# Kernel tuning notes

Hardware: AMD Instinct MI355X
Metric: run time of the kernel (lower is better)

Reference implementation:

```python
import jax, jax.numpy as jnp
import numpy as np

ALPHA = 0.2  # LeakyReLU negative slope

def setup_inputs() -> dict:
    key = jax.random.key(0)
    k1, k2, k3 = jax.random.split(key, 3)
    B, N, IN_DIM = 16, 1024, 128
    HEADS, HEAD_DIM = 2, 64  # out_dim = 128
    h = jax.random.normal(k1, (B, N, IN_DIM), dtype=jnp.float32)
    # xavier_uniform with gain=1.414 ~ uniform(-b, b); exact init unimportant for correctness
    bW = 1.414 * np.sqrt(6.0 / (IN_DIM + HEAD_DIM))
    W = jax.random.uniform(k2, (HEADS, IN_DIM, HEAD_DIM), minval=-bW, maxval=bW, dtype=jnp.float32)
    ba = 1.414 * np.sqrt(6.0 / (2 * HEAD_DIM + 1))
    a = jax.random.uniform(k3, (HEADS, 2 * HEAD_DIM, 1), minval=-ba, maxval=ba, dtype=jnp.float32)
    return {"h": h, "W": W, "a": a}

def reference(h, W, a):
    B, N, in_dim = h.shape
    heads, _, head_dim = W.shape
    out_dim = heads * head_dim
    # h_prime: [B, N, H, D]
    hp = jnp.einsum('bni,hio->bnho', h, W)
    # Split additive attention: a . [h_i ; h_j] = a_src . h_i + a_dst . h_j (same math as concat)
    a_src = a[:, :head_dim, 0]   # [H, D]
    a_dst = a[:, head_dim:, 0]   # [H, D]
    e_src = jnp.einsum('bnhd,hd->bhn', hp, a_src)  # [B, H, N]
    e_dst = jnp.einsum('bmhd,hd->bhm', hp, a_dst)  # [B, H, N]
    e = e_src[:, :, :, None] + e_dst[:, :, None, :]  # [B, H, N, N]
    e = jnp.where(e >= 0, e, ALPHA * e)  # LeakyReLU(0.2)
    att = jax.nn.softmax(e, axis=-1)
    # dropout p=0.0 (eval-deterministic): no-op
    h_new = jnp.einsum('bhnm,bmho->bnho', att, hp).reshape(B, N, out_dim)
    out = h_new + h if in_dim == out_dim else h_new
    return jax.nn.elu(out)
```

## Files before the change

### kernel.cpp

```cpp
#include <hip/hip_runtime.h>
#include <math.h>


#define LOG2E 1.44269504088896340736f

typedef __bf16 bf16x8 __attribute__((ext_vector_type(8)));
typedef float floatx4 __attribute__((ext_vector_type(4)));

union U16x8 { uint4 u; bf16x8 b; };

__device__ __forceinline__ unsigned short f2bf(float f) {
    union { __bf16 b; unsigned short u; } x;
    x.b = (__bf16)f;
    return x.u;
}

__global__ __launch_bounds__(256) void gat_prep(
    const float* __restrict__ Wg,
    const float* __restrict__ ag,
    unsigned short* __restrict__ Wp,
    float* __restrict__ acat)
{
    const int t = threadIdx.x;
    const int base = blockIdx.x * 1024;
#pragma unroll
    for (int i = 0; i < 4; ++i) {
        int idx = base + i * 256 + t;
        int c = idx & 127, k = idx >> 7;
        float v = Wg[(c >> 6) * 8192 + k * 64 + (c & 63)];
        Wp[((k >> 3) * 128 + c) * 8 + (k & 7)] = f2bf(v);
    }
    if (blockIdx.x == 0 && t < 128) {
        acat[t]       = ag[(t >> 6) * 128 + (t & 63)];
        acat[128 + t] = ag[(t >> 6) * 128 + 64 + (t & 63)];
    }
}

__global__ __launch_bounds__(256) void gat_hp(
    const float* __restrict__ hg,
    const unsigned short* __restrict__ Wp,
    const float* __restrict__ acat,
    unsigned short* __restrict__ hpB,
    float* __restrict__ es_g,
    float* __restrict__ ed_g)
{
    const int t = threadIdx.x;
    const int lane = t & 63;
    const int wv = blockIdx.x * 4 + (t >> 6);
    const int rt = wv >> 1;
    const int half = wv & 1;
    const int n0 = rt * 16;
    const int col = lane & 15, quad = lane >> 4;

    floatx4 acc[4];
#pragma unroll
    for (int ct = 0; ct < 4; ++ct) acc[ct] = (floatx4){0.f, 0.f, 0.f, 0.f};

    const float* hrow = hg + (size_t)(n0 + col) * 128;
    const uint4* wp4 = (const uint4*)Wp;
#pragma unroll
    for (int kq = 0; kq < 4; ++kq) {
        float4 h0 = *(const float4*)(hrow + kq * 32 + quad * 8);
        float4 h1 = *(const float4*)(hrow + kq * 32 + quad * 8 + 4);
        bf16x8 af;
        af[0] = (__bf16)h0.x; af[1] = (__bf16)h0.y;
        af[2] = (__bf16)h0.z; af[3] = (__bf16)h0.w;
        af[4] = (__bf16)h1.x; af[5] = (__bf16)h1.y;
        af[6] = (__bf16)h1.z; af[7] = (__bf16)h1.w;
        const uint4* wbase = wp4 + (size_t)(kq * 4 + quad) * 128 + half * 64;
#pragma unroll
        for (int ct = 0; ct < 4; ++ct) {
            U16x8 bu; bu.u = wbase[ct * 16 + col];
            acc[ct] = __builtin_amdgcn_mfma_f32_16x16x32_bf16(af, bu.b, acc[ct], 0, 0, 0);
        }
    }

    const int b = n0 >> 10;
    const int nloc = n0 & 1023;
    const int bh = b * 2 + half;

    float esr[4] = {0.f, 0.f, 0.f, 0.f}, edr[4] = {0.f, 0.f, 0.f, 0.f};
#pragma unroll
    for (int ct = 0; ct < 4; ++ct) {
        int c = half * 64 + ct * 16 + col;
        float as = acat[c], ad = acat[128 + c];
#pragma unroll
        for (int r = 0; r < 4; ++r) {
            esr[r] = fmaf(acc[ct][r], as, esr[r]);
            edr[r] = fmaf(acc[ct][r], ad, edr[r]);
        }
    }
#pragma unroll
    for (int off = 1; off <= 8; off <<= 1) {
#pragma unroll
        for (int r = 0; r < 4; ++r) {
            esr[r] += __shfl_xor(esr[r], off, 64);
            edr[r] += __shfl_xor(edr[r], off, 64);
        }
    }
    if (col == 0) {
        size_t base = (size_t)bh * 1024 + nloc + quad * 4;
#pragma unroll
        for (int r = 0; r < 4; ++r) {
            es_g[base + r] = esr[r];
            ed_g[base + r] = edr[r];
        }
    }

    const int gloc = (nloc >> 3) + (quad >> 1);
#pragma unroll
    for (int ct = 0; ct < 4; ++ct) {
        int d = ct * 16 + col;
        uint2 pk;
        pk.x = (unsigned)f2bf(acc[ct][0]) | ((unsigned)f2bf(acc[ct][1]) << 16);
        pk.y = (unsigned)f2bf(acc[ct][2]) | ((unsigned)f2bf(acc[ct][3]) << 16);
        size_t idx = ((size_t)(bh * 128 + gloc) * 64 + d) * 8 + (quad & 1) * 4;
        *(uint2*)(hpB + idx) = pk;
    }
}

__global__ __launch_bounds__(256, 2) void gat_att(
    const float* __restrict__ hg,
    const unsigned short* __restrict__ hpB,
    const float* __restrict__ es_g,
    const float* __restrict__ ed_g,
    float* __restrict__ out)
{
    __shared__ float red[4 * 64 * 35];

    const int t = threadIdx.x;
    const int lane = t & 63;
    const int w = t >> 6;
    const int bh = blockIdx.x & 31;
    const int nt = blockIdx.x >> 5;
    const int b = bh >> 1, hh = bh & 1;
    const int n0 = nt * 32;
    const int col = lane & 15, quad = lane >> 4;

    const float* edrow = ed_g + (size_t)bh * 1024;

    float mx = -1e30f;
#pragma unroll
    for (int i = 0; i < 4; ++i) {
        float4 v = *(const float4*)(edrow + lane * 16 + i * 4);
        mx = fmaxf(mx, fmaxf(fmaxf(v.x, v.y), fmaxf(v.z, v.w)));
    }
#pragma unroll
    for (int off = 1; off < 64; off <<= 1) mx = fmaxf(mx, __shfl_xor(mx, off, 64));
    const float mxl = mx * LOG2E;

    const float s2a = es_g[(size_t)bh * 1024 + n0 + col] * LOG2E;
    const float s2b = es_g[(size_t)bh * 1024 + n0 + 16 + col] * LOG2E;
    const float x0a = s2a + mxl, x0b = s2b + mxl;
    const float Ma = fmaxf(x0a, 0.2f * x0a), Mb = fmaxf(x0b, 0.2f * x0b);
    const float s2ma = s2a - Ma, s5ma = 0.2f * s2a - Ma;
    const float s2mb = s2b - Mb, s5mb = 0.2f * s2b - Mb;
    const float K = LOG2E, K5 = 0.2f * LOG2E;

    floatx4 acc0[4], acc1[4];
#pragma unroll
    for (int ct = 0; ct < 4; ++ct) {
        acc0[ct] = (floatx4){0.f, 0.f, 0.f, 0.f};
        acc1[ct] = (floatx4){0.f, 0.f, 0.f, 0.f};
    }
    float ls0 = 0.f, ls1 = 0.f;

    const uint4* hb = (const uint4*)hpB + (size_t)bh * 8192;
    const int mbase = w * 256;

    float4 d0 = *(const float4*)(edrow + mbase + quad * 8);
    float4 d1 = *(const float4*)(edrow + mbase + quad * 8 + 4);
    int gm = (mbase >> 3) + quad;
    uint4 bu0 = hb[gm * 64 + col];
    uint4 bu1 = hb[gm * 64 + 16 + col];
    uint4 bu2 = hb[gm * 64 + 32 + col];
    uint4 bu3 = hb[gm * 64 + 48 + col];

#pragma unroll
    for (int i = 0; i < 8; ++i) {
        float4 c0 = d0, c1 = d1;
        uint4 cb0 = bu0, cb1 = bu1, cb2 = bu2, cb3 = bu3;
        if (i < 7) {
            int m1 = mbase + (i + 1) * 32;
            d0 = *(const float4*)(edrow + m1 + quad * 8);
            d1 = *(const float4*)(edrow + m1 + quad * 8 + 4);
            gm = (m1 >> 3) + quad;
            bu0 = hb[gm * 64 + col];
            bu1 = hb[gm * 64 + 16 + col];
            bu2 = hb[gm * 64 + 32 + col];
            bu3 = hb[gm * 64 + 48 + col];
        }
        float dv[8] = {c0.x, c0.y, c0.z, c0.w, c1.x, c1.y, c1.z, c1.w};
        bf16x8 af0, af1;
#pragma unroll
        for (int j = 0; j < 8; ++j) {
            float pa = __builtin_amdgcn_exp2f(fmaxf(fmaf(dv[j], K, s2ma), fmaf(dv[j], K5, s5ma)));
            float pb = __builtin_amdgcn_exp2f(fmaxf(fmaf(dv[j], K, s2mb), fmaf(dv[j], K5, s5mb)));
            ls0 += pa; ls1 += pb;
            af0[j] = (__bf16)pa;
            af1[j] = (__bf16)pb;
        }
        U16x8 u0; u0.u = cb0;
        U16x8 u1; u1.u = cb1;
        U16x8 u2; u2.u = cb2;
        U16x8 u3; u3.u = cb3;
        acc0[0] = __builtin_amdgcn_mfma_f32_16x16x32_bf16(af0, u0.b, acc0[0], 0, 0, 0);
        acc1[0] = __builtin_amdgcn_mfma_f32_16x16x32_bf16(af1, u0.b, acc1[0], 0, 0, 0);
        acc0[1] = __builtin_amdgcn_mfma_f32_16x16x32_bf16(af0, u1.b, acc0[1], 0, 0, 0);
        acc1[1] = __builtin_amdgcn_mfma_f32_16x16x32_bf16(af1, u1.b, acc1[1], 0, 0, 0);
        acc0[2] = __builtin_amdgcn_mfma_f32_16x16x32_bf16(af0, u2.b, acc0[2], 0, 0, 0);
        acc1[2] = __builtin_amdgcn_mfma_f32_16x16x32_bf16(af1, u2.b, acc1[2], 0, 0, 0);
        acc0[3] = __builtin_amdgcn_mfma_f32_16x16x32_bf16(af0, u3.b, acc0[3], 0, 0, 0);
        acc1[3] = __builtin_amdgcn_mfma_f32_16x16x32_bf16(af1, u3.b, acc1[3], 0, 0, 0);
    }

    ls0 += __shfl_xor(ls0, 16, 64); ls0 += __shfl_xor(ls0, 32, 64);
    ls1 += __shfl_xor(ls1, 16, 64); ls1 += __shfl_xor(ls1, 32, 64);

    float* myred = red + (w * 64 + lane) * 35;
#pragma unroll
    for (int ct = 0; ct < 4; ++ct)
#pragma unroll
        for (int r = 0; r < 4; ++r) {
            myred[ct * 4 + r]      = acc0[ct][r];
            myred[16 + ct * 4 + r] = acc1[ct][r];
        }
    myred[32] = ls0;
    myred[33] = ls1;
    __syncthreads();

    const int tile = w & 1;
    const int ctp = w >> 1;
    float ltot = 0.f;
#pragma unroll
    for (int v4 = 0; v4 < 4; ++v4)
        ltot += red[(v4 * 64 + lane) * 35 + 32 + tile];
    float inv[4];
#pragma unroll
    for (int r = 0; r < 4; ++r)
        inv[r] = __builtin_amdgcn_rcpf(__shfl(ltot, quad * 4 + r, 16));

#pragma unroll
    for (int cti = 0; cti < 2; ++cti) {
        const int ct = ctp * 2 + cti;
        float facc[4] = {0.f, 0.f, 0.f, 0.f};
#pragma unroll
        for (int v4 = 0; v4 < 4; ++v4) {
            const float* rr = red + (v4 * 64 + lane) * 35 + tile * 16 + ct * 4;
#pragma unroll
            for (int r = 0; r < 4; ++r) facc[r] += rr[r];
        }
#pragma unroll
        for (int r = 0; r < 4; ++r) {
            int n = n0 + tile * 16 + quad * 4 + r;
            size_t off = (size_t)(b * 1024 + n) * 128 + hh * 64 + ct * 16 + col;
            float vv = facc[r] * inv[r] + hg[off];
            out[off] = vv > 0.f ? vv : __builtin_amdgcn_exp2f(vv * LOG2E) - 1.f;
        }
    }
}

extern "C" void kernel_launch(void* const* d_in, const int* in_sizes, int n_in,
                              void* d_out, int out_size, void* d_ws, size_t ws_size,
                              hipStream_t stream) {
    const float* h = (const float*)d_in[0];
    const float* W = (const float*)d_in[1];
    const float* a = (const float*)d_in[2];
    float* out = (float*)d_out;

    unsigned short* hpB = (unsigned short*)d_ws;
    float* es  = (float*)((char*)d_ws + (4u << 20));
    float* ed  = es + 32 * 1024;
    unsigned short* Wp = (unsigned short*)(ed + 32 * 1024);
    float* acat = (float*)((char*)Wp + 16384 * sizeof(unsigned short));

    gat_prep<<<16, 256, 0, stream>>>(W, a, Wp, acat);
    gat_hp<<<512, 256, 0, stream>>>(h, Wp, acat, hpB, es, ed);
    gat_att<<<1024, 256, 0, stream>>>(h, hpB, es, ed, out);
}
```

Before: 82.06 us.

## Fold attention vectors into W and split hp projection across more waves

Precomputes W·a_src and W·a_dst per head in the prep kernel, so the attention logits come straight from the fp32 input h with a dot product instead of a reduction over the bf16 MFMA outputs. The hp kernel now gives each wave two column tiles instead of four, doubling the grid to 1024 blocks for more parallelism and fewer accumulators per wave. Logits now use full-precision h rather than the bf16-rounded hp, which slightly changes the numerics. Rows of h are loaded twice, once by each column-pair wave.

```diff
diff --git a/kernel.cpp b/kernel.cpp
--- a/kernel.cpp
+++ b/kernel.cpp
@@ -19,7 +19,8 @@
     const float* __restrict__ Wg,
     const float* __restrict__ ag,
     unsigned short* __restrict__ Wp,
-    float* __restrict__ acat)
+    float* __restrict__ va_g,
+    float* __restrict__ vd_g)
 {
     const int t = threadIdx.x;
     const int base = blockIdx.x * 1024;
@@ -30,16 +31,28 @@
         float v = Wg[(c >> 6) * 8192 + k * 64 + (c & 63)];
         Wp[((k >> 3) * 128 + c) * 8 + (k & 7)] = f2bf(v);
     }
-    if (blockIdx.x == 0 && t < 128) {
-        acat[t]       = ag[(t >> 6) * 128 + (t & 63)];
-        acat[128 + t] = ag[(t >> 6) * 128 + 64 + (t & 63)];
+    if (blockIdx.x == 0) {
+        int head = t >> 7, k = t & 127;
+        const float* wrow = Wg + head * 8192 + k * 64;
+        const float* as = ag + head * 128;
+        const float* ad = as + 64;
+        float sa = 0.f, sd = 0.f;
+#pragma unroll
+        for (int d = 0; d < 64; ++d) {
+            float wv = wrow[d];
+            sa = fmaf(wv, as[d], sa);
+            sd = fmaf(wv, ad[d], sd);
+        }
+        va_g[head * 128 + k] = sa;
+        vd_g[head * 128 + k] = sd;
     }
 }
 
 __global__ __launch_bounds__(256) void gat_hp(
     const float* __restrict__ hg,
     const unsigned short* __restrict__ Wp,
-    const float* __restrict__ acat,
+    const float* __restrict__ va_g,
+    const float* __restrict__ vd_g,
     unsigned short* __restrict__ hpB,
     float* __restrict__ es_g,
     float* __restrict__ ed_g)
@@ -47,31 +60,48 @@
     const int t = threadIdx.x;
     const int lane = t & 63;
     const int wv = blockIdx.x * 4 + (t >> 6);
-    const int rt = wv >> 1;
-    const int half = wv & 1;
+    const int rt = wv >> 2;
+    const int half = (wv >> 1) & 1;
+    const int ctp = wv & 1;
     const int n0 = rt * 16;
     const int col = lane & 15, quad = lane >> 4;
 
-    floatx4 acc[4];
-#pragma unroll
-    for (int ct = 0; ct < 4; ++ct) acc[ct] = (floatx4){0.f, 0.f, 0.f, 0.f};
+    floatx4 acc[2];
+    acc[0] = (floatx4){0.f, 0.f, 0.f, 0.f};
+    acc[1] = (floatx4){0.f, 0.f, 0.f, 0.f};
+
+    float esr = 0.f, edr = 0.f;
+    const float* varow = va_g + half * 128;
+    const float* vdrow = vd_g + half * 128;
 
     const float* hrow = hg + (size_t)(n0 + col) * 128;
     const uint4* wp4 = (const uint4*)Wp;
 #pragma unroll
     for (int kq = 0; kq < 4; ++kq) {
-        float4 h0 = *(const float4*)(hrow + kq * 32 + quad * 8);
-        float4 h1 = *(const float4*)(hrow + kq * 32 + quad * 8 + 4);
+        const int k0 = kq * 32 + quad * 8;
+        float4 h0 = *(const float4*)(hrow + k0);
+        float4 h1 = *(const float4*)(hrow + k0 + 4);
         bf16x8 af;
         af[0] = (__bf16)h0.x; af[1] = (__bf16)h0.y;
         af[2] = (__bf16)h0.z; af[3] = (__bf16)h0.w;
         af[4] = (__bf16)h1.x; af[5] = (__bf16)h1.y;
         af[6] = (__bf16)h1.z; af[7] = (__bf16)h1.w;
-        const uint4* wbase = wp4 + (size_t)(kq * 4 + quad) * 128 + half * 64;
-#pragma unroll
-        for (int ct = 0; ct < 4; ++ct) {
-            U16x8 bu; bu.u = wbase[ct * 16 + col];
-            acc[ct] = __builtin_amdgcn_mfma_f32_16x16x32_bf16(af, bu.b, acc[ct], 0, 0, 0);
+        const uint4* wbase = wp4 + (size_t)(kq * 4 + quad) * 128 + half * 64 + ctp * 32;
+        {
+            U16x8 bu; bu.u = wbase[col];
+            acc[0] = __builtin_amdgcn_mfma_f32_16x16x32_bf16(af, bu.b, acc[0], 0, 0, 0);
+        }
+        {
+            U16x8 bu; bu.u = wbase[16 + col];
+            acc[1] = __builtin_amdgcn_mfma_f32_16x16x32_bf16(af, bu.b, acc[1], 0, 0, 0);
+        }
+        if (ctp == 0) {
+            float hv[8] = {h0.x, h0.y, h0.z, h0.w, h1.x, h1.y, h1.z, h1.w};
+#pragma unroll
+            for (int j = 0; j < 8; ++j) {
+                esr = fmaf(hv[j], varow[k0 + j], esr);
+                edr = fmaf(hv[j], vdrow[k0 + j], edr);
+            }
         }
     }
 
@@ -79,41 +109,23 @@
     const int nloc = n0 & 1023;
     const int bh = b * 2 + half;
 
-    float esr[4] = {0.f, 0.f, 0.f, 0.f}, edr[4] = {0.f, 0.f, 0.f, 0.f};
-#pragma unroll
-    for (int ct = 0; ct < 4; ++ct) {
-        int c = half * 64 + ct * 16 + col;
-        float as = acat[c], ad = acat[128 + c];
-#pragma unroll
-        for (int r = 0; r < 4; ++r) {
-            esr[r] = fmaf(acc[ct][r], as, esr[r]);
-            edr[r] = fmaf(acc[ct][r], ad, edr[r]);
-        }
-    }
-#pragma unroll
-    for (int off = 1; off <= 8; off <<= 1) {
-#pragma unroll
-        for (int r = 0; r < 4; ++r) {
-            esr[r] += __shfl_xor(esr[r], off, 64);
-            edr[r] += __shfl_xor(edr[r], off, 64);
-        }
-    }
-    if (col == 0) {
-        size_t base = (size_t)bh * 1024 + nloc + quad * 4;
-#pragma unroll
-        for (int r = 0; r < 4; ++r) {
-            es_g[base + r] = esr[r];
-            ed_g[base + r] = edr[r];
+    if (ctp == 0) {
+        esr += __shfl_xor(esr, 16, 64); esr += __shfl_xor(esr, 32, 64);
+        edr += __shfl_xor(edr, 16, 64); edr += __shfl_xor(edr, 32, 64);
+        if (quad == 0) {
+            size_t base = (size_t)bh * 1024 + nloc + col;
+            es_g[base] = esr;
+            ed_g[base] = edr;
         }
     }
 
     const int gloc = (nloc >> 3) + (quad >> 1);
 #pragma unroll
-    for (int ct = 0; ct < 4; ++ct) {
-        int d = ct * 16 + col;
+    for (int cti = 0; cti < 2; ++cti) {
+        int d = (ctp * 2 + cti) * 16 + col;
         uint2 pk;
-        pk.x = (unsigned)f2bf(acc[ct][0]) | ((unsigned)f2bf(acc[ct][1]) << 16);
-        pk.y = (unsigned)f2bf(acc[ct][2]) | ((unsigned)f2bf(acc[ct][3]) << 16);
+        pk.x = (unsigned)f2bf(acc[cti][0]) | ((unsigned)f2bf(acc[cti][1]) << 16);
+        pk.y = (unsigned)f2bf(acc[cti][2]) | ((unsigned)f2bf(acc[cti][3]) << 16);
         size_t idx = ((size_t)(bh * 128 + gloc) * 64 + d) * 8 + (quad & 1) * 4;
         *(uint2*)(hpB + idx) = pk;
     }
@@ -272,9 +284,10 @@
     float* es  = (float*)((char*)d_ws + (4u << 20));
     float* ed  = es + 32 * 1024;
     unsigned short* Wp = (unsigned short*)(ed + 32 * 1024);
-    float* acat = (float*)((char*)Wp + 16384 * sizeof(unsigned short));
-
-    gat_prep<<<16, 256, 0, stream>>>(W, a, Wp, acat);
-    gat_hp<<<512, 256, 0, stream>>>(h, Wp, acat, hpB, es, ed);
+    float* va  = (float*)((char*)Wp + 16384 * sizeof(unsigned short));
+    float* vd  = va + 256;
+
+    gat_prep<<<16, 256, 0, stream>>>(W, a, Wp, va, vd);
+    gat_hp<<<1024, 256, 0, stream>>>(h, Wp, va, vd, hpB, es, ed);
     gat_att<<<1024, 256, 0, stream>>>(h, hpB, es, ed, out);
 }
```

Result: slower. 86.33 us (+5.2%).

## Fuse prep, projection and attention into one cooperative kernel with grid sync

Applied to the files above, without the earlier changes.

Replaces the three-kernel chain with a single cooperative launch of 512 blocks. The blocks first compute the bf16 projection and the attention logits, reading W directly as fp32 instead of through a pre-packed buffer, then meet at a grid-wide barrier. After the barrier each block runs two attention tiles. This removes two kernel launches and the prep pass. In exchange it adds grid-sync overhead, uses half as many attention blocks, and issues strided, uncoalesced W loads in the projection phase. The old path stays as a fallback if the cooperative launch fails.

```diff
diff --git a/kernel.cpp b/kernel.cpp
--- a/kernel.cpp
+++ b/kernel.cpp
@@ -1,4 +1,5 @@
 #include <hip/hip_runtime.h>
+#include <hip/hip_cooperative_groups.h>
 #include <math.h>
 
 
@@ -15,11 +16,228 @@
     return x.u;
 }
 
-__global__ __launch_bounds__(256) void gat_prep(
+__global__ __launch_bounds__(256, 2) void gat_fused(
+    const float* __restrict__ hg,
     const float* __restrict__ Wg,
     const float* __restrict__ ag,
-    unsigned short* __restrict__ Wp,
-    float* __restrict__ acat)
+    unsigned short* __restrict__ hpB,
+    float* __restrict__ es_g,
+    float* __restrict__ ed_g,
+    float* __restrict__ out)
+{
+    __shared__ float red[4 * 64 * 17];
+
+    const int t = threadIdx.x;
+    const int lane = t & 63;
+    const int w = t >> 6;
+    const int col = lane & 15, quad = lane >> 4;
+    const int blk = blockIdx.x;
+
+    {
+        const int wv = blk * 4 + w;
+        const int rt = wv >> 1;
+        const int half = wv & 1;
+        const int n0 = rt * 16;
+
+        floatx4 acc[4];
+#pragma unroll
+        for (int ct = 0; ct < 4; ++ct) acc[ct] = (floatx4){0.f, 0.f, 0.f, 0.f};
+
+        const float* hrow = hg + (size_t)(n0 + col) * 128;
+        const float* wbase = Wg + half * 8192;
+#pragma unroll
+        for (int kq = 0; kq < 4; ++kq) {
+            const int k0 = kq * 32 + quad * 8;
+            float4 h0 = *(const float4*)(hrow + k0);
+            float4 h1 = *(const float4*)(hrow + k0 + 4);
+            bf16x8 af;
+            af[0] = (__bf16)h0.x; af[1] = (__bf16)h0.y;
+            af[2] = (__bf16)h0.z; af[3] = (__bf16)h0.w;
+            af[4] = (__bf16)h1.x; af[5] = (__bf16)h1.y;
+            af[6] = (__bf16)h1.z; af[7] = (__bf16)h1.w;
+#pragma unroll
+            for (int ct = 0; ct < 4; ++ct) {
+                const float* wc = wbase + (size_t)k0 * 64 + ct * 16 + col;
+                bf16x8 bf;
+#pragma unroll
+                for (int j = 0; j < 8; ++j) bf[j] = (__bf16)wc[j * 64];
+                acc[ct] = __builtin_amdgcn_mfma_f32_16x16x32_bf16(af, bf, acc[ct], 0, 0, 0);
+            }
+        }
+
+        const int b = n0 >> 10;
+        const int nloc = n0 & 1023;
+        const int bh = b * 2 + half;
+
+        float esr[4] = {0.f, 0.f, 0.f, 0.f}, edr[4] = {0.f, 0.f, 0.f, 0.f};
+#pragma unroll
+        for (int ct = 0; ct < 4; ++ct) {
+            int d = ct * 16 + col;
+            float as = ag[half * 128 + d];
+            float ad = ag[half * 128 + 64 + d];
+#pragma unroll
+            for (int r = 0; r < 4; ++r) {
+                esr[r] = fmaf(acc[ct][r], as, esr[r]);
+                edr[r] = fmaf(acc[ct][r], ad, edr[r]);
+            }
+        }
+#pragma unroll
+        for (int off = 1; off <= 8; off <<= 1) {
+#pragma unroll
+            for (int r = 0; r < 4; ++r) {
+                esr[r] += __shfl_xor(esr[r], off, 64);
+                edr[r] += __shfl_xor(edr[r], off, 64);
+            }
+        }
+        if (col == 0) {
+            size_t base = (size_t)bh * 1024 + nloc + quad * 4;
+#pragma unroll
+            for (int r = 0; r < 4; ++r) {
+                es_g[base + r] = esr[r];
+                ed_g[base + r] = edr[r];
+            }
+        }
+
+        const int gloc = (nloc >> 3) + (quad >> 1);
+#pragma unroll
+        for (int ct = 0; ct < 4; ++ct) {
+            int d = ct * 16 + col;
+            uint2 pk;
+            pk.x = (unsigned)f2bf(acc[ct][0]) | ((unsigned)f2bf(acc[ct][1]) << 16);
+            pk.y = (unsigned)f2bf(acc[ct][2]) | ((unsigned)f2bf(acc[ct][3]) << 16);
+            size_t idx = ((size_t)(bh * 128 + gloc) * 64 + d) * 8 + (quad & 1) * 4;
+            *(uint2*)(hpB + idx) = pk;
+        }
+    }
+
+    __threadfence();
+    cooperative_groups::this_grid().sync();
+
+    const int bh = blk & 31;
+    const int b = bh >> 1, hh = bh & 1;
+    const float* edrow = ed_g + (size_t)bh * 1024;
+    const uint4* hbb = (const uint4*)hpB + (size_t)bh * 8192;
+    const int mbase = w * 256;
+
+    float mx = -1e30f;
+#pragma unroll
+    for (int i = 0; i < 4; ++i) {
+        float4 v = *(const float4*)(edrow + lane * 16 + i * 4);
+        mx = fmaxf(mx, fmaxf(fmaxf(v.x, v.y), fmaxf(v.z, v.w)));
+    }
+#pragma unroll
+    for (int off = 1; off < 64; off <<= 1) mx = fmaxf(mx, __shfl_xor(mx, off, 64));
+    const float mxl = mx * LOG2E;
+    const float K = LOG2E, K5 = 0.2f * LOG2E;
+
+    for (int it = 0; it < 2; ++it) {
+        const int nt = (blk >> 5) + it * 16;
+        const int n0 = nt * 32;
+
+        const float s2a = es_g[(size_t)bh * 1024 + n0 + col] * LOG2E;
+        const float s2b = es_g[(size_t)bh * 1024 + n0 + 16 + col] * LOG2E;
+        const float x0a = s2a + mxl, x0b = s2b + mxl;
+        const float Ma = fmaxf(x0a, 0.2f * x0a), Mb = fmaxf(x0b, 0.2f * x0b);
+        const float s2ma = s2a - Ma, s5ma = 0.2f * s2a - Ma;
+        const float s2mb = s2b - Mb, s5mb = 0.2f * s2b - Mb;
+
+        floatx4 acc0[4], acc1[4];
+#pragma unroll
+        for (int ct = 0; ct < 4; ++ct) {
+            acc0[ct] = (floatx4){0.f, 0.f, 0.f, 0.f};
+            acc1[ct] = (floatx4){0.f, 0.f, 0.f, 0.f};
+        }
+        float ls0 = 0.f, ls1 = 0.f;
+
+        float4 d0 = *(const float4*)(edrow + mbase + quad * 8);
+        float4 d1 = *(const float4*)(edrow + mbase + quad * 8 + 4);
+        int gm = (mbase >> 3) + quad;
+        uint4 bu0 = hbb[gm * 64 + col];
+        uint4 bu1 = hbb[gm * 64 + 16 + col];
+        uint4 bu2 = hbb[gm * 64 + 32 + col];
+        uint4 bu3 = hbb[gm * 64 + 48 + col];
+
+#pragma unroll
+        for (int i = 0; i < 8; ++i) {
+            float4 c0 = d0, c1 = d1;
+            uint4 cb0 = bu0, cb1 = bu1, cb2 = bu2, cb3 = bu3;
+            if (i < 7) {
+                int m1 = mbase + (i + 1) * 32;
+                d0 = *(const float4*)(edrow + m1 + quad * 8);
+                d1 = *(const float4*)(edrow + m1 + quad * 8 + 4);
+                gm = (m1 >> 3) + quad;
+                bu0 = hbb[gm * 64 + col];
+                bu1 = hbb[gm * 64 + 16 + col];
+                bu2 = hbb[gm * 64 + 32 + col];
+                bu3 = hbb[gm * 64 + 48 + col];
+            }
+            float dv[8] = {c0.x, c0.y, c0.z, c0.w, c1.x, c1.y, c1.z, c1.w};
+            bf16x8 af0, af1;
+#pragma unroll
+            for (int j = 0; j < 8; ++j) {
+                float pa = __builtin_amdgcn_exp2f(fmaxf(fmaf(dv[j], K, s2ma), fmaf(dv[j], K5, s5ma)));
+                float pb = __builtin_amdgcn_exp2f(fmaxf(fmaf(dv[j], K, s2mb), fmaf(dv[j], K5, s5mb)));
+                ls0 += pa; ls1 += pb;
+                af0[j] = (__bf16)pa;
+                af1[j] = (__bf16)pb;
+            }
+            U16x8 u0; u0.u = cb0;
+            U16x8 u1; u1.u = cb1;
+            U16x8 u2; u2.u = cb2;
+            U16x8 u3; u3.u = cb3;
+            acc0[0] = __builtin_amdgcn_mfma_f32_16x16x32_bf16(af0, u0.b, acc0[0], 0, 0, 0);
+            acc1[0] = __builtin_amdgcn_mfma_f32_16x16x32_bf16(af1, u0.b, acc1[0], 0, 0, 0);
+            acc0[1] = __builtin_amdgcn_mfma_f32_16x16x32_bf16(af0, u1.b, acc0[1], 0, 0, 0);
+            acc1[1] = __builtin_amdgcn_mfma_f32_16x16x32_bf16(af1, u1.b, acc1[1], 0, 0, 0);
+            acc0[2] = __builtin_amdgcn_mfma_f32_16x16x32_bf16(af0, u2.b, acc0[2], 0, 0, 0);
+            acc1[2] = __builtin_amdgcn_mfma_f32_16x16x32_bf16(af1, u2.b, acc1[2], 0, 0, 0);
+            acc0[3] = __builtin_amdgcn_mfma_f32_16x16x32_bf16(af0, u3.b, acc0[3], 0, 0, 0);
+            acc1[3] = __builtin_amdgcn_mfma_f32_16x16x32_bf16(af1, u3.b, acc1[3], 0, 0, 0);
+        }
+
+        ls0 += __shfl_xor(ls0, 16, 64); ls0 += __shfl_xor(ls0, 32, 64);
+        ls1 += __shfl_xor(ls1, 16, 64); ls1 += __shfl_xor(ls1, 32, 64);
+
+        float* myred = red + (w * 64 + lane) * 17;
+#pragma unroll
+        for (int sub = 0; sub < 2; ++sub) {
+            __syncthreads();
+#pragma unroll
+            for (int ct = 0; ct < 4; ++ct)
+#pragma unroll
+                for (int r = 0; r < 4; ++r)
+                    myred[ct * 4 + r] = (sub == 0) ? acc0[ct][r] : acc1[ct][r];
+            myred[16] = (sub == 0) ? ls0 : ls1;
+            __syncthreads();
+
+            float facc[4] = {0.f, 0.f, 0.f, 0.f};
+            float ltot = 0.f;
+#pragma unroll
+            for (int v4 = 0; v4 < 4; ++v4) {
+                const float* rr = red + (v4 * 64 + lane) * 17;
+#pragma unroll
+                for (int r = 0; r < 4; ++r) facc[r] += rr[w * 4 + r];
+                ltot += rr[16];
+            }
+            float inv[4];
+#pragma unroll
+            for (int r = 0; r < 4; ++r)
+                inv[r] = __builtin_amdgcn_rcpf(__shfl(ltot, quad * 4 + r, 16));
+
+#pragma unroll
+            for (int r = 0; r < 4; ++r) {
+                int n = n0 + sub * 16 + quad * 4 + r;
+                size_t off = (size_t)(b * 1024 + n) * 128 + hh * 64 + w * 16 + col;
+                float vv = facc[r] * inv[r] + hg[off];
+                out[off] = vv > 0.f ? vv : __builtin_amdgcn_exp2f(vv * LOG2E) - 1.f;
+            }
+        }
+    }
+}
+
+__global__ __launch_bounds__(256) void gat_prep(
+    const float* __restrict__ Wg, const float* __restrict__ ag,
+    unsigned short* __restrict__ Wp, float* __restrict__ acat)
 {
     const int t = threadIdx.x;
     const int base = blockIdx.x * 1024;
@@ -37,12 +255,9 @@
 }
 
 __global__ __launch_bounds__(256) void gat_hp(
-    const float* __restrict__ hg,
-    const unsigned short* __restrict__ Wp,
-    const float* __restrict__ acat,
-    unsigned short* __restrict__ hpB,
-    float* __restrict__ es_g,
-    float* __restrict__ ed_g)
+    const float* __restrict__ hg, const unsigned short* __restrict__ Wp,
+    const float* __restrict__ acat, unsigned short* __restrict__ hpB,
+    float* __restrict__ es_g, float* __restrict__ ed_g)
 {
     const int t = threadIdx.x;
     const int lane = t & 63;
@@ -120,10 +335,8 @@
 }
 
 __global__ __launch_bounds__(256, 2) void gat_att(
-    const float* __restrict__ hg,
-    const unsigned short* __restrict__ hpB,
-    const float* __restrict__ es_g,
-    const float* __restrict__ ed_g,
+    const float* __restrict__ hg, const unsigned short* __restrict__ hpB,
+    const float* __restrict__ es_g, const float* __restrict__ ed_g,
     float* __restrict__ out)
 {
     __shared__ float red[4 * 64 * 35];
@@ -274,7 +487,13 @@
     unsigned short* Wp = (unsigned short*)(ed + 32 * 1024);
     float* acat = (float*)((char*)Wp + 16384 * sizeof(unsigned short));
 
-    gat_prep<<<16, 256, 0, stream>>>(W, a, Wp, acat);
-    gat_hp<<<512, 256, 0, stream>>>(h, Wp, acat, hpB, es, ed);
-    gat_att<<<1024, 256, 0, stream>>>(h, hpB, es, ed, out);
-}
+    void* args[] = {(void*)&h, (void*)&W, (void*)&a,
+                    (void*)&hpB, (void*)&es, (void*)&ed, (void*)&out};
+    hipError_t e = hipLaunchCooperativeKernel((const void*)gat_fused,
+                                              dim3(512), dim3(256), args, 0, stream);
+    if (e != hipSuccess) {
+        gat_prep<<<16, 256, 0, stream>>>(W, a, Wp, acat);
+        gat_hp<<<512, 256, 0, stream>>>(h, Wp, acat, hpB, es, ed);
+        gat_att<<<1024, 256, 0, stream>>>(h, hpB, es, ed, out);
+    }
+}
```

Result: slower. 178.7 us (+117.7%).
